# Kernel optimization log

Hardware: AMD Instinct MI355X
Metric: run time of the kernel (lower is better)

The kernel has to match this reference:

```python
import jax, jax.numpy as jnp
import numpy as np
from jax import lax

NEG = -1.0e30  # finite stand-in for -inf (keeps vjp NaN-free)


def _ctc_losses(log_probs, input_lengths, targets, target_lengths, blank=0):
    """Per-sequence CTC negative log-likelihood (Graves 2006 forward algorithm).

    log_probs: (B,T,V) log-softmax outputs; targets: (B,U) padded labels (no blanks).
    Matches torch.nn.functional.ctc_loss(..., reduction='none') semantics per sequence.
    """
    B, T, V = log_probs.shape
    U = targets.shape[1]
    S = 2 * U + 1
    s = jnp.arange(S)
    tgt_idx = jnp.clip((s - 1) // 2, 0, U - 1)
    # Blank-interleaved extended label sequence: b, y1, b, y2, ..., yU, b
    ext = jnp.where((s % 2) == 0, blank, targets[:, tgt_idx])  # (B,S)
    ext_m2 = jnp.concatenate([jnp.full((B, 2), blank, ext.dtype), ext[:, :-2]], axis=1)
    can_skip = (ext != blank) & (ext != ext_m2) & (s >= 2)[None, :]
    idx = jnp.broadcast_to(ext[:, None, :], (B, T, S))
    lp_ext = jnp.take_along_axis(log_probs, idx, axis=2)  # (B,T,S)

    alpha0 = jnp.full((B, S), NEG, log_probs.dtype)
    alpha0 = alpha0.at[:, 0].set(lp_ext[:, 0, 0]).at[:, 1].set(lp_ext[:, 0, 1])
    neg1 = jnp.full((B, 1), NEG, log_probs.dtype)
    neg2 = jnp.full((B, 2), NEG, log_probs.dtype)

    def step(alpha, inp):
        lp_t, t = inp
        a1 = jnp.concatenate([neg1, alpha[:, :-1]], axis=1)
        a2 = jnp.concatenate([neg2, alpha[:, :-2]], axis=1)
        a2 = jnp.where(can_skip, a2, NEG)
        new = jnp.logaddexp(jnp.logaddexp(alpha, a1), a2) + lp_t
        # freeze alpha once past this sequence's input length
        alpha = jnp.where((t < input_lengths)[:, None], new, alpha)
        return alpha, None

    lp_seq = jnp.transpose(lp_ext[:, 1:, :], (1, 0, 2))  # (T-1,B,S)
    alpha, _ = lax.scan(step, alpha0, (lp_seq, jnp.arange(1, T)))
    end = 2 * target_lengths  # index of final blank in extended sequence
    a_blank = jnp.take_along_axis(alpha, end[:, None], axis=1)[:, 0]
    a_label = jnp.take_along_axis(alpha, jnp.maximum(end - 1, 0)[:, None], axis=1)[:, 0]
    return -jnp.logaddexp(a_blank, a_label)  # (B,)


def setup_inputs() -> dict:
    key = jax.random.key(0)
    k1, k2, k3, k4, k5, k6 = jax.random.split(key, 6)
    N, T, C, V, U = 16, 1000, 512, 2000, 100
    # Two augmented views of the same N utterances, stacked along batch (cr-ctc)
    enc_half = jax.random.normal(k1, (N, T, C), dtype=jnp.float32)
    encoder_out = jnp.concatenate(
        [enc_half, enc_half + 0.1 * jax.random.normal(k2, (N, T, C), dtype=jnp.float32)], axis=0)
    lens_half = jax.random.randint(k3, (N,), T // 2, T + 1, dtype=jnp.int32)
    encoder_out_lens = jnp.concatenate([lens_half, lens_half])
    tgt_half = jax.random.randint(k4, (N, U), 1, V, dtype=jnp.int32)  # labels in [1,V), 0 = blank
    targets = jnp.concatenate([tgt_half, tgt_half], axis=0)
    tl_half = jax.random.randint(k5, (N,), U // 2, U + 1, dtype=jnp.int32)
    target_lengths = jnp.concatenate([tl_half, tl_half])
    W = jax.random.normal(k6, (V, C), dtype=jnp.float32) * np.float32(1.0 / np.sqrt(C))
    b = jnp.zeros((V,), dtype=jnp.float32)
    return {"encoder_out": encoder_out, "W": W, "b": b,
            "encoder_out_lens": encoder_out_lens, "targets": targets,
            "target_lengths": target_lengths}


def reference(encoder_out, W, b, encoder_out_lens, targets, target_lengths):
    # ctc_output head: (Dropout is identity in eval) Linear -> LogSoftmax
    B, T, C = encoder_out.shape
    logits = jnp.einsum('btc,vc->btv', encoder_out, W) + b
    log_probs = jax.nn.log_softmax(logits, axis=-1)  # (B,T,V)
    # CTC loss, reduction='sum'
    ctc_loss = jnp.sum(_ctc_losses(log_probs, encoder_out_lens, targets, target_lengths))
    # Consistency regularization: KL(input=log p || target=log q), log_target=True,
    # q = detached log-probs of the swapped batch halves
    half = B // 2
    q = lax.stop_gradient(jnp.concatenate([log_probs[half:], log_probs[:half]], axis=0))
    kl = jnp.exp(q) * (q - log_probs)
    pad = (jnp.arange(T)[None, :] >= encoder_out_lens[:, None])[:, :, None]  # make_pad_mask
    cr_loss = jnp.sum(jnp.where(pad, 0.0, kl))
    return (0.5 * ctc_loss, 0.5 * cr_loss)
```

## Files before the change

### kernel.cpp

```cpp
#include <hip/hip_runtime.h>
#include <hip/hip_bf16.h>
#include <cstdint>

#define NEG (-1.0e30f)
#define INVLN2 1.44269504088896340736f
#define LN2    0.69314718055994530942f

typedef unsigned short u16;
typedef __attribute__((ext_vector_type(8))) short short8;
typedef __attribute__((ext_vector_type(4))) float f32x4;

typedef const __attribute__((address_space(1))) void cg_void;
typedef __attribute__((address_space(3))) void lds_void;

#define Bsz   32
#define Tlen  1000
#define Cdim  512
#define Vdim  2000
#define Udim  100
#define Mrows (Bsz * Tlen)
#define Npad  2048
#define GROW  256

#define WS_ABF 0u
#define WS_G   0u
#define WS_WBF 32768000u
#define WS_KL  WS_WBF
#define WS_Z   (WS_WBF + 2097152u)
#define WS_ACC (WS_Z + 128000000u)

__device__ inline u16 f2bf(float x) {
  uint32_t u = __float_as_uint(x);
  uint32_t r = (u + 0x7fffu + ((u >> 16) & 1u)) >> 16;
  return (u16)r;
}
__device__ inline float bf2f(u16 u) {
  return __uint_as_float(((uint32_t)u) << 16);
}

#define DPP_MAX_STAGE(m, ctrl) { \
    int _r = __builtin_amdgcn_update_dpp(__float_as_int(m), __float_as_int(m), \
                                         ctrl, 0xF, 0xF, false); \
    m = fmaxf(m, __int_as_float(_r)); }
#define DPP_SUM_STAGE(v, ctrl) { \
    int _r = __builtin_amdgcn_update_dpp(0, __float_as_int(v), \
                                         ctrl, 0xF, 0xF, true); \
    v += __int_as_float(_r); }

__device__ inline float dppMax64(float m) {
  DPP_MAX_STAGE(m, 0x111) DPP_MAX_STAGE(m, 0x112) DPP_MAX_STAGE(m, 0x114)
  DPP_MAX_STAGE(m, 0x118) DPP_MAX_STAGE(m, 0x142) DPP_MAX_STAGE(m, 0x143)
  return m;
}
__device__ inline float dppSum64(float v) {
  DPP_SUM_STAGE(v, 0x111) DPP_SUM_STAGE(v, 0x112) DPP_SUM_STAGE(v, 0x114)
  DPP_SUM_STAGE(v, 0x118) DPP_SUM_STAGE(v, 0x142) DPP_SUM_STAGE(v, 0x143)
  return v;
}

__device__ inline float shiftup1(float x, float fill) {
  int r = __builtin_amdgcn_update_dpp(__float_as_int(fill), __float_as_int(x),
                                      0x138, 0xF, 0xF, false);
  return __int_as_float(r);
}

__global__ void convert_kernel(const float4* __restrict__ enc4, const float4* __restrict__ W4,
                               uint4* __restrict__ a4, uint4* __restrict__ w4,
                               float* __restrict__ accum) {
  int idx = blockIdx.x * blockDim.x + threadIdx.x;
  int stride = gridDim.x * blockDim.x;
  if (idx == 0) { accum[0] = 0.0f; accum[1] = 0.0f; }
  const int nA = Mrows * Cdim / 8;
  const int nW = Vdim * Cdim / 8;
  const int nWp = Npad * Cdim / 8;
  for (int i = idx; i < nA; i += stride) {
    float4 x = enc4[2 * i], y = enc4[2 * i + 1];
    uint4 o;
    o.x = (uint32_t)f2bf(x.x) | ((uint32_t)f2bf(x.y) << 16);
    o.y = (uint32_t)f2bf(x.z) | ((uint32_t)f2bf(x.w) << 16);
    o.z = (uint32_t)f2bf(y.x) | ((uint32_t)f2bf(y.y) << 16);
    o.w = (uint32_t)f2bf(y.z) | ((uint32_t)f2bf(y.w) << 16);
    a4[i] = o;
  }
  for (int i = idx; i < nWp; i += stride) {
    uint4 o = {0, 0, 0, 0};
    if (i < nW) {
      float4 x = W4[2 * i], y = W4[2 * i + 1];
      o.x = (uint32_t)f2bf(x.x) | ((uint32_t)f2bf(x.y) << 16);
      o.y = (uint32_t)f2bf(x.z) | ((uint32_t)f2bf(x.w) << 16);
      o.z = (uint32_t)f2bf(y.x) | ((uint32_t)f2bf(y.y) << 16);
      o.w = (uint32_t)f2bf(y.z) | ((uint32_t)f2bf(y.w) << 16);
    }
    w4[i] = o;
  }
}

__global__ __launch_bounds__(256) void gemm_kernel(const u16* __restrict__ A,
                                                   const u16* __restrict__ Wb,
                                                   u16* __restrict__ Z) {
  __shared__ __attribute__((aligned(16))) u16 As[128 * 64];
  __shared__ __attribute__((aligned(16))) u16 Bs[128 * 64];
  const int tid = threadIdx.x;
  const int wave = tid >> 6;
  const int lane = tid & 63;
  const int nBase = blockIdx.x * 128;
  const int mBase = blockIdx.y * 128;
  const int m_lane = lane & 15;
  const int quad = lane >> 4;

  f32x4 acc[4][4];
  const f32x4 zero4 = {0.0f, 0.0f, 0.0f, 0.0f};
  #pragma unroll
  for (int i = 0; i < 4; ++i)
    #pragma unroll
    for (int j = 0; j < 4; ++j) acc[i][j] = zero4;

  for (int k0 = 0; k0 < Cdim; k0 += 64) {
    #pragma unroll
    for (int r = 0; r < 4; ++r) {
      int u = r * 256 + tid;
      int g = u >> 3;
      int q = (u & 7) ^ (g & 7);
      const u16* gpA = A + ((size_t)(mBase + g) << 9) + (k0 + (q << 3));
      __builtin_amdgcn_global_load_lds((cg_void*)gpA, (lds_void*)&As[(r * 4 + wave) * 512],
                                       16, 0, 0);
      const u16* gpB = Wb + ((size_t)(nBase + g) << 9) + (k0 + (q << 3));
      __builtin_amdgcn_global_load_lds((cg_void*)gpB, (lds_void*)&Bs[(r * 4 + wave) * 512],
                                       16, 0, 0);
    }
    __syncthreads();
    #pragma unroll
    for (int kk = 0; kk < 2; ++kk) {
      short8 af[4], bfv[4];
      #pragma unroll
      for (int mi = 0; mi < 4; ++mi) {
        int row = (wave >> 1) * 64 + mi * 16 + m_lane;
        int q = (kk * 4 + quad) ^ (row & 7);
        af[mi] = *(const short8*)&As[row * 64 + (q << 3)];
      }
      #pragma unroll
      for (int ni = 0; ni < 4; ++ni) {
        int col = (wave & 1) * 64 + ni * 16 + m_lane;
        int q = (kk * 4 + quad) ^ (col & 7);
        bfv[ni] = *(const short8*)&Bs[col * 64 + (q << 3)];
      }
      #pragma unroll
      for (int mi = 0; mi < 4; ++mi)
        #pragma unroll
        for (int ni = 0; ni < 4; ++ni)
          acc[mi][ni] = __builtin_amdgcn_mfma_f32_16x16x32_bf16(af[mi], bfv[ni],
                                                                acc[mi][ni], 0, 0, 0);
    }
    __syncthreads();
  }
  #pragma unroll
  for (int ni = 0; ni < 4; ++ni) {
    int col = nBase + (wave & 1) * 64 + ni * 16 + m_lane;
    if (col < Vdim) {
      #pragma unroll
      for (int mi = 0; mi < 4; ++mi) {
        int row0 = mBase + (wave >> 1) * 64 + mi * 16 + quad * 4;
        #pragma unroll
        for (int rg = 0; rg < 4; ++rg)
          Z[(size_t)(row0 + rg) * Vdim + col] = f2bf(acc[mi][ni][rg]);
      }
    }
  }
}

__global__ __launch_bounds__(256) void cr_stats_kernel(const u16* __restrict__ Z,
                                                       const float* __restrict__ bias,
                                                       const int* __restrict__ lens,
                                                       const int* __restrict__ targets,
                                                       const int* __restrict__ tlens,
                                                       float* __restrict__ G,
                                                       float* __restrict__ klp) {
  int bp = blockIdx.x;
  int t = blockIdx.y;
  int tid = threadIdx.x;
  size_t r1 = (size_t)bp * Tlen + t;
  if (t >= lens[bp]) {
    if (tid == 0) klp[r1] = 0.0f;
    return;
  }
  int wave = tid >> 6, lane = tid & 63;
  size_t r2 = r1 + (size_t)16 * Tlen;
  const u16* z1 = Z + r1 * Vdim;
  const u16* z2 = Z + r2 * Vdim;

  __shared__ __attribute__((aligned(16))) float ls1[Vdim];
  __shared__ __attribute__((aligned(16))) float ls2[Vdim];
  __shared__ float red[8];

  const int c0 = tid * 8;
  float v1[8], v2[8], e1[8], e2[8];
  float mx1 = NEG, mx2 = NEG;
  if (c0 < Vdim) {
    short8 za = *(const short8*)&z1[c0];
    short8 zb = *(const short8*)&z2[c0];
    float4 b0 = *(const float4*)&bias[c0];
    float4 b1 = *(const float4*)&bias[c0 + 4];
    float bb[8] = {b0.x, b0.y, b0.z, b0.w, b1.x, b1.y, b1.z, b1.w};
    #pragma unroll
    for (int j = 0; j < 8; ++j) {
      v1[j] = bf2f((u16)za[j]) + bb[j];
      v2[j] = bf2f((u16)zb[j]) + bb[j];
      mx1 = fmaxf(mx1, v1[j]);
      mx2 = fmaxf(mx2, v2[j]);
    }
    *(float4*)&ls1[c0]     = (float4){v1[0], v1[1], v1[2], v1[3]};
    *(float4*)&ls1[c0 + 4] = (float4){v1[4], v1[5], v1[6], v1[7]};
    *(float4*)&ls2[c0]     = (float4){v2[0], v2[1], v2[2], v2[3]};
    *(float4*)&ls2[c0 + 4] = (float4){v2[4], v2[5], v2[6], v2[7]};
  } else {
    #pragma unroll
    for (int j = 0; j < 8; ++j) { v1[j] = NEG; v2[j] = NEG; }
  }
  float w1 = dppMax64(mx1), w2 = dppMax64(mx2);
  if (lane == 63) { red[wave] = w1; red[4 + wave] = w2; }
  __syncthreads();
  float M1 = fmaxf(fmaxf(red[0], red[1]), fmaxf(red[2], red[3]));
  float M2 = fmaxf(fmaxf(red[4], red[5]), fmaxf(red[6], red[7]));
  __syncthreads();
  float s1 = 0.0f, s2 = 0.0f;
  #pragma unroll
  for (int j = 0; j < 8; ++j) {
    e1[j] = expf(v1[j] - M1);
    e2[j] = expf(v2[j] - M2);
    s1 += e1[j];
    s2 += e2[j];
  }
  s1 = dppSum64(s1); s2 = dppSum64(s2);
  if (lane == 63) { red[wave] = s1; red[4 + wave] = s2; }
  __syncthreads();
  float S1 = red[0] + red[1] + red[2] + red[3];
  float S2 = red[4] + red[5] + red[6] + red[7];
  float c1 = M1 + logf(S1);
  float c2 = M2 + logf(S2);
  float inv1 = 1.0f / S1;
  float inv2 = 1.0f / S2;

  if (tid < 64) {
    int i1 = min(2 * tid, Udim - 1);
    int i3 = min(2 * tid + 1, Udim - 1);
    int t1a = targets[bp * Udim + i1];
    int t1b = targets[bp * Udim + i3];
    int t2a = targets[(bp + 16) * Udim + i1];
    int t2b = targets[(bp + 16) * Udim + i3];
    int tl1 = tlens[bp];
    int tl2 = tlens[bp + 16];
    float4 g1 = {(2 * tid < tl1) ? expf(ls1[t1a] - c1) : 0.0f,
                 (2 * tid + 1 < tl1) ? expf(ls1[t1b] - c1) : 0.0f,
                 expf(ls1[0] - c1), 0.0f};
    float4 g2 = {(2 * tid < tl2) ? expf(ls2[t2a] - c2) : 0.0f,
                 (2 * tid + 1 < tl2) ? expf(ls2[t2b] - c2) : 0.0f,
                 expf(ls2[0] - c2), 0.0f};
    *(float4*)(G + r1 * GROW + 4 * tid) = g1;
    *(float4*)(G + r2 * GROW + 4 * tid) = g2;
  }

  float f = 0.0f;
  #pragma unroll
  for (int j = 0; j < 8; ++j) {
    float p1 = e1[j] * inv1;
    float p2 = e2[j] * inv2;
    f += (p1 - p2) * (v1[j] - v2[j]);
  }
  __syncthreads();
  f = dppSum64(f);
  if (lane == 63) red[wave] = f;
  __syncthreads();
  if (tid == 0) {
    klp[r1] = red[0] + red[1] + red[2] + red[3];
  }
}

#define DECL3(p, i) float p##i##x, p##i##y, p##i##b;
#define LOADR(p, i, row) { float4 v = *(const float4*)(gb + (size_t)(row) * GROW + 4 * lane); \
    p##i##x = v.x; p##i##y = v.y; p##i##b = v.z; }

#define COMPU(p, i) { \
    float pX = p##i##x, pY = p##i##y, pB = p##i##b; \
    float p3 = shiftup1(a3, 0.0f); \
    float t01 = a1 + a0; \
    float t23 = a3 + a2; \
    float n0 = (a0 + p3) * pB; \
    float n1 = fmaf(p3, fm1, t01) * pX; \
    float n2 = (a2 + a1) * pB; \
    float n3 = fmaf(a1, fm3, t23) * pY; \
    a0 = n0; a1 = n1; a2 = n2; a3 = n3; }

#define COMPA(p, i, off) { \
    float pX = p##i##x, pY = p##i##y, pB = p##i##b; \
    float p3 = shiftup1(a3, 0.0f); \
    float t01 = a1 + a0; \
    float t23 = a3 + a2; \
    float n0 = (a0 + p3) * pB; \
    float n1 = fmaf(p3, fm1, t01) * pX; \
    float n2 = (a2 + a1) * pB; \
    float n3 = fmaf(a1, fm3, t23) * pY; \
    bool act = (t + (off)) < len; \
    a0 = act ? n0 : a0; a1 = act ? n1 : a1; \
    a2 = act ? n2 : a2; a3 = act ? n3 : a3; }

#define DPPMAX(m, ctrl) { int _r = __builtin_amdgcn_update_dpp(0,              \
      __float_as_int(m), ctrl, 0xF, 0xF, true);                               \
    m = fmaxf(m, __int_as_float(_r)); }

#define RESCALE_KILL(tdone) {                                                 \
    int R = len - 1 - (tdone); R = R < 0 ? 0 : R;                             \
    int lo = end1 - 2 * R;                                                    \
    a0 = (base4 + 0 >= lo) ? a0 : 0.0f;                                       \
    a1 = (base4 + 1 >= lo) ? a1 : 0.0f;                                       \
    a2 = (base4 + 2 >= lo) ? a2 : 0.0f;                                       \
    a3 = (base4 + 3 >= lo) ? a3 : 0.0f;                                       \
    float m = fmaxf(fmaxf(a0, a1), fmaxf(a2, a3));                            \
    DPPMAX(m, 0x111) DPPMAX(m, 0x112) DPPMAX(m, 0x114) DPPMAX(m, 0x118)       \
    DPPMAX(m, 0x142) DPPMAX(m, 0x143)                                         \
    uint32_t mb = (uint32_t)__builtin_amdgcn_readlane(__float_as_int(m), 63); \
    int e = (int)((mb >> 23) & 0xffu);                                        \
    int sh = 227 - e;                                                         \
    sh = sh > 127 ? 127 : (sh < -126 ? -126 : sh);                            \
    float sc = __uint_as_float((uint32_t)(sh + 127) << 23);                   \
    a0 *= sc; a1 *= sc; a2 *= sc; a3 *= sc;                                   \
    logScale -= sh; }

__global__ __launch_bounds__(64, 1) void ctc_kernel(const float* __restrict__ G,
                                                    const int* __restrict__ targets,
                                                    const int* __restrict__ lens,
                                                    const int* __restrict__ tlens,
                                                    float* __restrict__ accum) {
  int b = blockIdx.x;
  int lane = threadIdx.x;
  const int* tgt = targets + b * Udim;
  int i1 = min(2 * lane, Udim - 1);
  int i3 = min(2 * lane + 1, Udim - 1);
  int l1 = tgt[i1];
  int l3 = tgt[i3];
  int lm1 = tgt[min(max(2 * lane - 1, 0), Udim - 1)];
  const float fm1 = ((lane >= 1) && (l1 != lm1)) ? 1.0f : 0.0f;
  const float fm3 = (l3 != l1) ? 1.0f : 0.0f;
  int len = lens[b];
  int tl = tlens[b];
  const int end1 = 2 * tl - 1;
  const int base4 = 4 * lane;
  const float* gb = G + (size_t)b * Tlen * GROW;

  float4 v0 = *(const float4*)(gb + 4 * lane);
  float a0 = (lane == 0) ? v0.z : 0.0f;
  float a1 = (lane == 0) ? v0.x : 0.0f;
  float a2 = 0.0f, a3 = 0.0f;
  int logScale = 0;

  DECL3(sA, 0)  DECL3(sA, 1)  DECL3(sA, 2)  DECL3(sA, 3)
  DECL3(sA, 4)  DECL3(sA, 5)  DECL3(sA, 6)  DECL3(sA, 7)
  DECL3(sA, 8)  DECL3(sA, 9)  DECL3(sA, 10) DECL3(sA, 11)
  DECL3(sA, 12) DECL3(sA, 13) DECL3(sA, 14) DECL3(sA, 15)
  DECL3(sB, 0)  DECL3(sB, 1)  DECL3(sB, 2)  DECL3(sB, 3)
  DECL3(sB, 4)  DECL3(sB, 5)  DECL3(sB, 6)  DECL3(sB, 7)
  DECL3(sB, 8)  DECL3(sB, 9)  DECL3(sB, 10) DECL3(sB, 11)
  DECL3(sB, 12) DECL3(sB, 13) DECL3(sB, 14) DECL3(sB, 15)

  LOADR(sA, 0, 1)   LOADR(sA, 1, 2)   LOADR(sA, 2, 3)   LOADR(sA, 3, 4)
  LOADR(sA, 4, 5)   LOADR(sA, 5, 6)   LOADR(sA, 6, 7)   LOADR(sA, 7, 8)
  LOADR(sA, 8, 9)   LOADR(sA, 9, 10)  LOADR(sA, 10, 11) LOADR(sA, 11, 12)
  LOADR(sA, 12, 13) LOADR(sA, 13, 14) LOADR(sA, 14, 15) LOADR(sA, 15, 16)

  int steps = len - 1;
  int mainN = steps & ~31;
  int t = 1;
  for (int blk = 0; blk < mainN; blk += 32) {
    LOADR(sB, 0, t + 16)  LOADR(sB, 1, t + 17)  LOADR(sB, 2, t + 18)  LOADR(sB, 3, t + 19)
    LOADR(sB, 4, t + 20)  LOADR(sB, 5, t + 21)  LOADR(sB, 6, t + 22)  LOADR(sB, 7, t + 23)
    LOADR(sB, 8, t + 24)  LOADR(sB, 9, t + 25)  LOADR(sB, 10, t + 26) LOADR(sB, 11, t + 27)
    LOADR(sB, 12, t + 28) LOADR(sB, 13, t + 29) LOADR(sB, 14, t + 30) LOADR(sB, 15, t + 31)
    __builtin_amdgcn_sched_barrier(0);
    COMPU(sA, 0)  COMPU(sA, 1)  COMPU(sA, 2)  COMPU(sA, 3)
    COMPU(sA, 4)  COMPU(sA, 5)  COMPU(sA, 6)  COMPU(sA, 7)
    RESCALE_KILL(t + 7)
    COMPU(sA, 8)  COMPU(sA, 9)  COMPU(sA, 10) COMPU(sA, 11)
    COMPU(sA, 12) COMPU(sA, 13) COMPU(sA, 14) COMPU(sA, 15)
    RESCALE_KILL(t + 15)
    LOADR(sA, 0, t + 32)  LOADR(sA, 1, t + 33)  LOADR(sA, 2, t + 34)  LOADR(sA, 3, t + 35)
    LOADR(sA, 4, t + 36)  LOADR(sA, 5, t + 37)  LOADR(sA, 6, t + 38)  LOADR(sA, 7, t + 39)
    LOADR(sA, 8, t + 40)  LOADR(sA, 9, t + 41)  LOADR(sA, 10, t + 42) LOADR(sA, 11, t + 43)
    LOADR(sA, 12, t + 44) LOADR(sA, 13, t + 45) LOADR(sA, 14, t + 46) LOADR(sA, 15, t + 47)
    __builtin_amdgcn_sched_barrier(0);
    COMPU(sB, 0)  COMPU(sB, 1)  COMPU(sB, 2)  COMPU(sB, 3)
    COMPU(sB, 4)  COMPU(sB, 5)  COMPU(sB, 6)  COMPU(sB, 7)
    RESCALE_KILL(t + 23)
    COMPU(sB, 8)  COMPU(sB, 9)  COMPU(sB, 10) COMPU(sB, 11)
    COMPU(sB, 12) COMPU(sB, 13) COMPU(sB, 14) COMPU(sB, 15)
    RESCALE_KILL(t + 31)
    t += 32;
  }
  {
    LOADR(sB, 0, t + 16)  LOADR(sB, 1, t + 17)  LOADR(sB, 2, t + 18)  LOADR(sB, 3, t + 19)
    LOADR(sB, 4, t + 20)  LOADR(sB, 5, t + 21)  LOADR(sB, 6, t + 22)  LOADR(sB, 7, t + 23)
    LOADR(sB, 8, t + 24)  LOADR(sB, 9, t + 25)  LOADR(sB, 10, t + 26) LOADR(sB, 11, t + 27)
    LOADR(sB, 12, t + 28) LOADR(sB, 13, t + 29) LOADR(sB, 14, t + 30) LOADR(sB, 15, t + 31)
    __builtin_amdgcn_sched_barrier(0);
    COMPA(sA, 0, 0)   COMPA(sA, 1, 1)   COMPA(sA, 2, 2)   COMPA(sA, 3, 3)
    COMPA(sA, 4, 4)   COMPA(sA, 5, 5)   COMPA(sA, 6, 6)   COMPA(sA, 7, 7)
    RESCALE_KILL(t + 7)
    COMPA(sA, 8, 8)   COMPA(sA, 9, 9)   COMPA(sA, 10, 10) COMPA(sA, 11, 11)
    COMPA(sA, 12, 12) COMPA(sA, 13, 13) COMPA(sA, 14, 14) COMPA(sA, 15, 15)
    RESCALE_KILL(t + 15)
    COMPA(sB, 0, 16)  COMPA(sB, 1, 17)  COMPA(sB, 2, 18)  COMPA(sB, 3, 19)
    COMPA(sB, 4, 20)  COMPA(sB, 5, 21)  COMPA(sB, 6, 22)  COMPA(sB, 7, 23)
    RESCALE_KILL(t + 23)
    COMPA(sB, 8, 24)  COMPA(sB, 9, 25)  COMPA(sB, 10, 26) COMPA(sB, 11, 27)
    COMPA(sB, 12, 28) COMPA(sB, 13, 29) COMPA(sB, 14, 30) COMPA(sB, 15, 31)
    RESCALE_KILL(t + 31)
  }

  __shared__ float fin[256];
  fin[4 * lane + 0] = a0;
  fin[4 * lane + 1] = a1;
  fin[4 * lane + 2] = a2;
  fin[4 * lane + 3] = a3;
  __syncthreads();
  if (lane == 0) {
    int end = 2 * tl;
    float sum = fin[end] + fin[end - 1];
    float loss = -LN2 * (log2f(sum) + (float)logScale);
    atomicAdd(&accum[0], 0.5f * loss);
  }
}

__global__ __launch_bounds__(1024) void finalize_kernel(const float* __restrict__ accum,
                                                        const float* __restrict__ klp,
                                                        float* __restrict__ out) {
  __shared__ float red[16];
  int tid = threadIdx.x;
  float s = 0.0f;
  for (int i = tid; i < 16 * Tlen; i += 1024) s += klp[i];
  s = dppSum64(s);
  int wave = tid >> 6, lane = tid & 63;
  if (lane == 63) red[wave] = s;
  __syncthreads();
  if (tid == 0) {
    float tot = 0.0f;
    #pragma unroll
    for (int w = 0; w < 16; ++w) tot += red[w];
    out[0] = accum[0];
    out[1] = 0.5f * tot;
  }
}

extern "C" void kernel_launch(void* const* d_in, const int* in_sizes, int n_in,
                              void* d_out, int out_size, void* d_ws, size_t ws_size,
                              hipStream_t stream) {
  const float* enc = (const float*)d_in[0];
  const float* W = (const float*)d_in[1];
  const float* bias = (const float*)d_in[2];
  const int* lens = (const int*)d_in[3];
  const int* targets = (const int*)d_in[4];
  const int* tlens = (const int*)d_in[5];

  char* ws = (char*)d_ws;
  u16* a_bf = (u16*)(ws + WS_ABF);
  u16* w_bf = (u16*)(ws + WS_WBF);
  u16* Zb   = (u16*)(ws + WS_Z);
  float* Gp  = (float*)(ws + WS_G);
  float* klp = (float*)(ws + WS_KL);
  float* accum = (float*)(ws + WS_ACC);

  hipLaunchKernelGGL(convert_kernel, dim3(1024), dim3(256), 0, stream,
                     (const float4*)enc, (const float4*)W, (uint4*)a_bf, (uint4*)w_bf, accum);
  hipLaunchKernelGGL(gemm_kernel, dim3(16, 250), dim3(256), 0, stream,
                     a_bf, w_bf, Zb);
  hipLaunchKernelGGL(cr_stats_kernel, dim3(16, 1000), dim3(256), 0, stream,
                     Zb, bias, lens, targets, tlens, Gp, klp);
  hipLaunchKernelGGL(ctc_kernel, dim3(Bsz), dim3(64), 0, stream,
                     Gp, targets, lens, tlens, accum);
  hipLaunchKernelGGL(finalize_kernel, dim3(1), dim3(1024), 0, stream,
                     accum, klp, (float*)d_out);
}
```

Baseline: 306.1 us.

## Skip padded rows in convert and GEMM, remap GEMM tiles for L2 locality

The convert kernel now skips bf16 conversion of encoder rows past each sequence's length. The GEMM drops tiles whose rows are all padding and switches to a 1D grid with a grouped tile ordering (8 M-tiles per group) meant to improve L2 reuse of A and W. Rows of A that are skipped hold stale data, so partially padded tiles still compute on garbage, and the downstream kernels have to ignore those rows. Whole tiles skipped this way leave Z uninitialised for their rows, which is only safe if cr_stats and ctc never read them.

```diff
diff --git a/kernel.cpp b/kernel.cpp
--- a/kernel.cpp
+++ b/kernel.cpp
@@ -66,6 +66,7 @@
 
 __global__ void convert_kernel(const float4* __restrict__ enc4, const float4* __restrict__ W4,
                                uint4* __restrict__ a4, uint4* __restrict__ w4,
+                               const int* __restrict__ lens,
                                float* __restrict__ accum) {
   int idx = blockIdx.x * blockDim.x + threadIdx.x;
   int stride = gridDim.x * blockDim.x;
@@ -74,6 +75,10 @@
   const int nW = Vdim * Cdim / 8;
   const int nWp = Npad * Cdim / 8;
   for (int i = idx; i < nA; i += stride) {
+    int row = i >> 6;
+    int b = row / 1000;
+    int t = row - b * 1000;
+    if (t >= lens[b]) continue;
     float4 x = enc4[2 * i], y = enc4[2 * i + 1];
     uint4 o;
     o.x = (uint32_t)f2bf(x.x) | ((uint32_t)f2bf(x.y) << 16);
@@ -97,14 +102,26 @@
 
 __global__ __launch_bounds__(256) void gemm_kernel(const u16* __restrict__ A,
                                                    const u16* __restrict__ Wb,
+                                                   const int* __restrict__ lens,
                                                    u16* __restrict__ Z) {
+  const int id = blockIdx.x;
+  const int c = id >> 7, r = id & 127;
+  int mTile, nTile;
+  if (c < 31) { mTile = c * 8 + (r & 7); nTile = r >> 3; }
+  else        { mTile = 248 + (r & 1);   nTile = r >> 1; }
+  const int mBase = mTile * 128;
+  const int nBase = nTile * 128;
+  {
+    int bSeq = mBase / 1000;
+    int t0 = mBase - bSeq * 1000;
+    if (t0 <= 872 && t0 >= lens[bSeq]) return;
+  }
+
   __shared__ __attribute__((aligned(16))) u16 As[128 * 64];
   __shared__ __attribute__((aligned(16))) u16 Bs[128 * 64];
   const int tid = threadIdx.x;
   const int wave = tid >> 6;
   const int lane = tid & 63;
-  const int nBase = blockIdx.x * 128;
-  const int mBase = blockIdx.y * 128;
   const int m_lane = lane & 15;
   const int quad = lane >> 4;
 
@@ -117,15 +134,15 @@
 
   for (int k0 = 0; k0 < Cdim; k0 += 64) {
     #pragma unroll
-    for (int r = 0; r < 4; ++r) {
-      int u = r * 256 + tid;
+    for (int rr = 0; rr < 4; ++rr) {
+      int u = rr * 256 + tid;
       int g = u >> 3;
       int q = (u & 7) ^ (g & 7);
       const u16* gpA = A + ((size_t)(mBase + g) << 9) + (k0 + (q << 3));
-      __builtin_amdgcn_global_load_lds((cg_void*)gpA, (lds_void*)&As[(r * 4 + wave) * 512],
+      __builtin_amdgcn_global_load_lds((cg_void*)gpA, (lds_void*)&As[(rr * 4 + wave) * 512],
                                        16, 0, 0);
       const u16* gpB = Wb + ((size_t)(nBase + g) << 9) + (k0 + (q << 3));
-      __builtin_amdgcn_global_load_lds((cg_void*)gpB, (lds_void*)&Bs[(r * 4 + wave) * 512],
+      __builtin_amdgcn_global_load_lds((cg_void*)gpB, (lds_void*)&Bs[(rr * 4 + wave) * 512],
                                        16, 0, 0);
     }
     __syncthreads();
@@ -467,9 +484,10 @@
   float* accum = (float*)(ws + WS_ACC);
 
   hipLaunchKernelGGL(convert_kernel, dim3(1024), dim3(256), 0, stream,
-                     (const float4*)enc, (const float4*)W, (uint4*)a_bf, (uint4*)w_bf, accum);
-  hipLaunchKernelGGL(gemm_kernel, dim3(16, 250), dim3(256), 0, stream,
-                     a_bf, w_bf, Zb);
+                     (const float4*)enc, (const float4*)W, (uint4*)a_bf, (uint4*)w_bf,
+                     lens, accum);
+  hipLaunchKernelGGL(gemm_kernel, dim3(4000), dim3(256), 0, stream,
+                     a_bf, w_bf, lens, Zb);
   hipLaunchKernelGGL(cr_stats_kernel, dim3(16, 1000), dim3(256), 0, stream,
                      Zb, bias, lens, targets, tlens, Gp, klp);
   hipLaunchKernelGGL(ctc_kernel, dim3(Bsz), dim3(64), 0, stream,
```

Measured after the change: 289.7 us. 5.3% less time.
